# Kernel tuning notes

Hardware: AMD Instinct MI355X
Metric: run time of the kernel (lower is better)

Reference implementation:

```python
import jax, jax.numpy as jnp
import numpy as np

B, C, H, W = 128, 2048, 11, 11
BN_EPS = 1e-5
STEEPNESS = 10.0


def setup_inputs() -> dict:
    key = jax.random.key(0)
    ks = jax.random.split(key, 4)
    x = jax.random.normal(ks[0], (B, C, H, W), dtype=jnp.float32)
    freq_threshold = jnp.full((1, C, 1, 1), 0.25, dtype=jnp.float32)
    gate = jnp.full((1,), 0.1, dtype=jnp.float32)
    # kaiming normal fan_out for 1x1 conv: std = sqrt(2 / fan_out), fan_out = C*1*1
    conv_w = jax.random.normal(ks[1], (C, C), dtype=jnp.float32) * np.sqrt(2.0 / C).astype(np.float32)
    conv_b = jnp.zeros((C,), dtype=jnp.float32)
    bn_gamma = jnp.ones((C,), dtype=jnp.float32)
    bn_beta = jnp.zeros((C,), dtype=jnp.float32)
    bn_mean = jnp.zeros((C,), dtype=jnp.float32)
    bn_var = jnp.ones((C,), dtype=jnp.float32)
    return {
        "x": x, "freq_threshold": freq_threshold, "gate": gate,
        "conv_w": conv_w, "conv_b": conv_b,
        "bn_gamma": bn_gamma, "bn_beta": bn_beta,
        "bn_mean": bn_mean, "bn_var": bn_var,
    }


def _hp_mask(cutoff, h, w, dtype):
    # radial distance from the (shifted) DC bin, normalized by max corner distance
    cy, cx = h // 2, w // 2
    yy = (jnp.arange(h, dtype=dtype) - cy)[:, None]
    xx = (jnp.arange(w, dtype=dtype) - cx)[None, :]
    dist = jnp.sqrt(yy ** 2 + xx ** 2)
    max_dist = jnp.sqrt(jnp.asarray(cy ** 2 + cx ** 2, dtype=dtype))
    dn = dist / (max_dist + 1e-6)  # [H, W]
    return jax.nn.sigmoid(STEEPNESS * (dn[None, None] - cutoff))  # [1, C, H, W]


def reference(x, freq_threshold, gate, conv_w, conv_b, bn_gamma, bn_beta, bn_mean, bn_var):
    # FFT -> shifted high-pass mask -> iFFT (real part)
    x_freq = jnp.fft.fftshift(jnp.fft.fft2(x, norm="ortho"), axes=(-2, -1))
    cutoff = jnp.clip(freq_threshold, 0.05, 0.5)
    mask = _hp_mask(cutoff, x.shape[-2], x.shape[-1], x.dtype)
    x_filt = jnp.fft.ifft2(jnp.fft.ifftshift(x_freq * mask, axes=(-2, -1)), norm="ortho").real
    # refine: 1x1 conv + BN (inference stats) + ReLU
    y = jnp.einsum("bchw,oc->bohw", x_filt, conv_w) + conv_b[None, :, None, None]
    inv = (bn_gamma / jnp.sqrt(bn_var + BN_EPS))[None, :, None, None]
    y = (y - bn_mean[None, :, None, None]) * inv + bn_beta[None, :, None, None]
    y = jax.nn.relu(y)
    g = jnp.clip(gate, 0.0, 1.0)
    return x + g * y
```

## Files before the change

### kernel.cpp

```cpp
#include <hip/hip_runtime.h>
#include <cstdint>
#include <cstddef>


#define C_DIM 2048
#define HW 121
#define NB 128
#define NTOT (NB * HW)

__device__ __forceinline__ unsigned short f2bf(float f) {
  union { float f; unsigned int u; } v;
  v.f = f;
  unsigned int r = (v.u + 0x7FFFu + ((v.u >> 16) & 1u)) >> 16;
  return (unsigned short)r;
}

typedef __bf16 bfrag __attribute__((ext_vector_type(8)));
typedef float f32x4 __attribute__((ext_vector_type(4)));
typedef float f32x2 __attribute__((ext_vector_type(2)));

__device__ __forceinline__ void gload_lds16(const void* g, void* l) {
  __builtin_amdgcn_global_load_lds(
      (const __attribute__((address_space(1))) unsigned int*)(uintptr_t)g,
      (__attribute__((address_space(3))) unsigned int*)(uintptr_t)l, 16, 0, 0);
}

__global__ __launch_bounds__(256) void prep_kernel(
    const float* __restrict__ ft, const float* __restrict__ convb,
    const float* __restrict__ gamma, const float* __restrict__ beta,
    const float* __restrict__ mean, const float* __restrict__ var,
    float* __restrict__ kws, float* __restrict__ alpha,
    float* __restrict__ beta2) {
  __shared__ float msk[121];
  __shared__ float ctab[11];
  const int c = blockIdx.x;
  const int t = threadIdx.x;
  float cutoff = ft[c];
  cutoff = fminf(fmaxf(cutoff, 0.05f), 0.5f);
  if (t < 121) {
    int h = t / 11, w = t - (t / 11) * 11;
    float dy = (float)(h - 5), dx = (float)(w - 5);
    float dn = sqrtf(dy * dy + dx * dx) / (sqrtf(50.0f) + 1e-6f);
    msk[t] = 1.0f / (1.0f + expf(-10.0f * (dn - cutoff)));
  }
  if (t < 11) ctab[t] = cosf(6.283185307179586f * (float)t / 11.0f);
  if (t == 128) {
    float inv = gamma[c] * rsqrtf(var[c] + 1e-5f);
    alpha[c] = inv;
    beta2[c] = (convb[c] - mean[c]) * inv + beta[c];
  }
  __syncthreads();
  if (t < 176) {
    int h = t >> 4, w = t & 15;
    float val = 0.0f;
    if (w < 11) {
      float acc = 0.0f;
      int ru = 0;
      int us = 5;
      for (int u = 0; u < 11; u++) {
        int rv = ru;
        int vs = 5;
        for (int v = 0; v < 11; v++) {
          acc += msk[us * 11 + vs] * ctab[rv];
          rv += w; if (rv >= 11) rv -= 11;
          vs++; if (vs >= 11) vs -= 11;
        }
        ru += h; if (ru >= 11) ru -= 11;
        us++; if (us >= 11) us -= 11;
      }
      val = acc * (1.0f / 121.0f);
    }
    kws[(size_t)c * 176 + t] = val;
  }
}

__global__ __launch_bounds__(256) void wconv_kernel(
    const float* __restrict__ W, unsigned short* __restrict__ Wb) {
  int idx = (blockIdx.x * 256 + threadIdx.x) * 8;
  float4 a = *(const float4*)(W + idx);
  float4 b = *(const float4*)(W + idx + 4);
  union { unsigned short s[8]; uint4 v; } u;
  u.s[0] = f2bf(a.x); u.s[1] = f2bf(a.y); u.s[2] = f2bf(a.z); u.s[3] = f2bf(a.w);
  u.s[4] = f2bf(b.x); u.s[5] = f2bf(b.y); u.s[6] = f2bf(b.z); u.s[7] = f2bf(b.w);
  *(uint4*)(Wb + idx) = u.v;
}

#define XROW 12
#define XPL 132
__global__ __launch_bounds__(704) void filter_kernel(
    const float* __restrict__ x, const float* __restrict__ kws,
    unsigned short* __restrict__ xf) {
  __shared__ __align__(16) float lx[64 * XPL];
  const int b = blockIdx.x;
  const int c0 = blockIdx.y * 64;
  const int tid = threadIdx.x;

  const float* xsrc = x + ((size_t)b * C_DIM + c0) * HW;
#pragma unroll
  for (int i = 0; i < 11; i++) {
    int g = tid + i * 704;
    int pl = g / 121;
    int r = g - pl * 121;
    int rh = r / 11;
    int rw = r - rh * 11;
    lx[pl * XPL + rh * XROW + rw] = xsrc[g];
  }
  __syncthreads();

  const int pl = tid / 11;
  const int ph = tid - pl * 11;
  const float* xp = &lx[pl * XPL];
  const float* kp = kws + (size_t)(c0 + pl) * 176;

  f32x2 acc2[6];
#pragma unroll
  for (int i = 0; i < 6; i++) acc2[i] = f32x2{0.f, 0.f};

  for (int kh = 0; kh < 11; kh++) {
    int qh = ph - kh; if (qh < 0) qh += 11;
    f32x4 xv0 = *(const f32x4*)(xp + qh * XROW);
    f32x4 xv1 = *(const f32x4*)(xp + qh * XROW + 4);
    f32x4 xv2 = *(const f32x4*)(xp + qh * XROW + 8);
    f32x4 kv0 = *(const f32x4*)(kp + kh * 16);
    f32x4 kv1 = *(const f32x4*)(kp + kh * 16 + 4);
    f32x4 kv2 = *(const f32x4*)(kp + kh * 16 + 8);
    const float xr[11] = {xv0[0], xv0[1], xv0[2], xv0[3], xv1[0], xv1[1],
                          xv1[2], xv1[3], xv2[0], xv2[1], xv2[2]};
    float kr[12];
    kr[0] = kv0[0]; kr[1] = kv0[1]; kr[2] = kv0[2]; kr[3] = kv0[3];
    kr[4] = kv1[0]; kr[5] = kv1[1]; kr[6] = kv1[2]; kr[7] = kv1[3];
    kr[8] = kv2[0]; kr[9] = kv2[1]; kr[10] = kv2[2];
    kr[11] = kr[0];
#pragma unroll
    for (int qw = 0; qw < 11; qw++) {
      f32x2 xv = {xr[qw], xr[qw]};
#pragma unroll
      for (int p2 = 0; p2 < 6; p2++) {
        int ki = 2 * p2 - qw; if (ki < 0) ki += 11;
        f32x2 kpair = {kr[ki], kr[ki + 1]};
        acc2[p2] = xv * kpair + acc2[p2];
      }
    }
  }
  __syncthreads();

  float accv[11];
#pragma unroll
  for (int p2 = 0; p2 < 6; p2++) {
    accv[2 * p2] = acc2[p2][0];
    if (2 * p2 + 1 < 11) accv[2 * p2 + 1] = acc2[p2][1];
  }

  unsigned short* lo = (unsigned short*)lx;
#pragma unroll
  for (int pw = 0; pw < 11; pw++)
    lo[(ph * 11 + pw) * 64 + pl] = f2bf(accv[pw]);
  __syncthreads();

  const unsigned int* lou = (const unsigned int*)lo;
#pragma unroll
  for (int i = 0; i < 6; i++) {
    int idx = tid + i * 704;
    if (idx < 3872) {
      int p = idx >> 5;
      int j = idx & 31;
      ((unsigned int*)(xf + (size_t)(b * HW + p) * C_DIM + c0))[j] = lou[idx];
    }
  }
}

__global__ __launch_bounds__(256) void gemm_kernel(
    const unsigned short* __restrict__ Wb, const unsigned short* __restrict__ xf,
    const float* __restrict__ xres, const float* __restrict__ alpha,
    const float* __restrict__ beta2, const float* __restrict__ gate,
    float* __restrict__ out) {
  __shared__ __align__(16) unsigned short lds[16384];
  const int tid = threadIdx.x;
  const int wid = tid >> 6;
  const int lane = tid & 63;

  const int lid = blockIdx.y * 121 + blockIdx.x;
  const int grp = lid / 176;
  const int rem = lid - grp * 176;
  const int m0 = (rem & 15) << 7;
  const int n0 = (grp * 11 + (rem >> 4)) << 7;

  const int wm = (wid >> 1) << 6;
  const int wn = (wid & 1) << 6;

  f32x4 acc[4][4];
#pragma unroll
  for (int i = 0; i < 4; i++)
#pragma unroll
    for (int j = 0; j < 4; j++) acc[i][j] = f32x4{0.f, 0.f, 0.f, 0.f};

  const int rowlo = (wid << 4) + (lane >> 2);
  const int seg = lane & 3;
  const unsigned short* gA0 = Wb + (size_t)(m0 + rowlo) * C_DIM + seg * 8;
  const unsigned short* gA1 = gA0 + 64 * C_DIM;
  const unsigned short* gB0 = xf + (size_t)(n0 + rowlo) * C_DIM + seg * 8;
  const unsigned short* gB1 = gB0 + 64 * C_DIM;
  char* lA0 = (char*)lds + (wid << 10) + (lane << 4);
  char* lA1 = lA0 + 4096;

  const int fr = lane & 15;
  const int quad = lane >> 4;
  const unsigned short* pa = lds + ((wm + fr) << 5) + (quad << 3);
  const unsigned short* pb = lds + 8192 + ((wn + fr) << 5) + (quad << 3);

  for (int kk = 0; kk < 32; kk++) {
    gload_lds16(gA0,       lA0);
    gload_lds16(gA1,       lA1);
    gload_lds16(gA0 + 32,  lA0 + 8192);
    gload_lds16(gA1 + 32,  lA1 + 8192);
    gload_lds16(gB0,       lA0 + 16384);
    gload_lds16(gB1,       lA1 + 16384);
    gload_lds16(gB0 + 32,  lA0 + 24576);
    gload_lds16(gB1 + 32,  lA1 + 24576);
    gA0 += 64; gA1 += 64; gB0 += 64; gB1 += 64;
    asm volatile("s_waitcnt vmcnt(0)" ::: "memory");
    __syncthreads();
#pragma unroll
    for (int ks = 0; ks < 2; ks++) {
      bfrag a[4], b[4];
#pragma unroll
      for (int i = 0; i < 4; i++) {
        a[i] = *(const bfrag*)(pa + (ks << 12) + (i << 9));
        b[i] = *(const bfrag*)(pb + (ks << 12) + (i << 9));
      }
#pragma unroll
      for (int i = 0; i < 4; i++)
#pragma unroll
        for (int j = 0; j < 4; j++)
          acc[i][j] = __builtin_amdgcn_mfma_f32_16x16x32_bf16(a[i], b[j], acc[i][j], 0, 0, 0);
    }
    __syncthreads();
  }

  float g = gate[0];
  g = fminf(fmaxf(g, 0.0f), 1.0f);
  int nbase[4];
#pragma unroll
  for (int j = 0; j < 4; j++) {
    int n = n0 + wn + (j << 4) + fr;
    int bb = n / 121;
    int p = n - bb * 121;
    nbase[j] = bb * (C_DIM * HW) + p;
  }
#pragma unroll
  for (int i = 0; i < 4; i++) {
    const int ob = m0 + wm + (i << 4) + (quad << 2);
    float al[4], bt[4];
#pragma unroll
    for (int r = 0; r < 4; r++) { al[r] = alpha[ob + r]; bt[r] = beta2[ob + r]; }
#pragma unroll
    for (int j = 0; j < 4; j++) {
#pragma unroll
      for (int r = 0; r < 4; r++) {
        int addr = nbase[j] + (ob + r) * HW;
        float v = acc[i][j][r] * al[r] + bt[r];
        v = fmaxf(v, 0.0f);
        out[addr] = xres[addr] + g * v;
      }
    }
  }
}

extern "C" void kernel_launch(void* const* d_in, const int* in_sizes, int n_in,
                              void* d_out, int out_size, void* d_ws, size_t ws_size,
                              hipStream_t stream) {
  const float* x     = (const float*)d_in[0];
  const float* ft    = (const float*)d_in[1];
  const float* gate  = (const float*)d_in[2];
  const float* W     = (const float*)d_in[3];
  const float* convb = (const float*)d_in[4];
  const float* gamma = (const float*)d_in[5];
  const float* beta  = (const float*)d_in[6];
  const float* mean  = (const float*)d_in[7];
  const float* var   = (const float*)d_in[8];
  float* out = (float*)d_out;

  char* ws = (char*)d_ws;
  float* kws            = (float*)(ws);
  float* alpha          = (float*)(ws + 0x200000);
  float* beta2          = (float*)(ws + 0x202000);
  unsigned short* Wb    = (unsigned short*)(ws + 0x300000);
  unsigned short* xf    = (unsigned short*)(ws + 0xC00000);

  prep_kernel<<<2048, 256, 0, stream>>>(ft, convb, gamma, beta, mean, var,
                                        kws, alpha, beta2);
  wconv_kernel<<<2048, 256, 0, stream>>>(W, Wb);
  filter_kernel<<<dim3(NB, C_DIM / 64), 704, 0, stream>>>(x, kws, xf);
  gemm_kernel<<<dim3(NTOT / 128, C_DIM / 128), 256, 0, stream>>>(
      Wb, xf, x, alpha, beta2, gate, out);
}
```

Baseline: 535.3 us.

## Fold weight conversion into prep, exploit kernel symmetry in circular filter

```diff
diff --git a/kernel.cpp b/kernel.cpp
--- a/kernel.cpp
+++ b/kernel.cpp
@@ -17,7 +17,6 @@
 
 typedef __bf16 bfrag __attribute__((ext_vector_type(8)));
 typedef float f32x4 __attribute__((ext_vector_type(4)));
-typedef float f32x2 __attribute__((ext_vector_type(2)));
 
 __device__ __forceinline__ void gload_lds16(const void* g, void* l) {
   __builtin_amdgcn_global_load_lds(
@@ -29,12 +28,24 @@
     const float* __restrict__ ft, const float* __restrict__ convb,
     const float* __restrict__ gamma, const float* __restrict__ beta,
     const float* __restrict__ mean, const float* __restrict__ var,
+    const float* __restrict__ W, unsigned short* __restrict__ Wb,
     float* __restrict__ kws, float* __restrict__ alpha,
     float* __restrict__ beta2) {
   __shared__ float msk[121];
   __shared__ float ctab[11];
   const int c = blockIdx.x;
   const int t = threadIdx.x;
+
+  {
+    int base = c * C_DIM + t * 8;
+    float4 a = *(const float4*)(W + base);
+    float4 b = *(const float4*)(W + base + 4);
+    union { unsigned short s[8]; uint4 v; } u;
+    u.s[0] = f2bf(a.x); u.s[1] = f2bf(a.y); u.s[2] = f2bf(a.z); u.s[3] = f2bf(a.w);
+    u.s[4] = f2bf(b.x); u.s[5] = f2bf(b.y); u.s[6] = f2bf(b.z); u.s[7] = f2bf(b.w);
+    *(uint4*)(Wb + base) = u.v;
+  }
+
   float cutoff = ft[c];
   cutoff = fminf(fmaxf(cutoff, 0.05f), 0.5f);
   if (t < 121) {
@@ -74,96 +85,89 @@
   }
 }
 
-__global__ __launch_bounds__(256) void wconv_kernel(
-    const float* __restrict__ W, unsigned short* __restrict__ Wb) {
-  int idx = (blockIdx.x * 256 + threadIdx.x) * 8;
-  float4 a = *(const float4*)(W + idx);
-  float4 b = *(const float4*)(W + idx + 4);
-  union { unsigned short s[8]; uint4 v; } u;
-  u.s[0] = f2bf(a.x); u.s[1] = f2bf(a.y); u.s[2] = f2bf(a.z); u.s[3] = f2bf(a.w);
-  u.s[4] = f2bf(b.x); u.s[5] = f2bf(b.y); u.s[6] = f2bf(b.z); u.s[7] = f2bf(b.w);
-  *(uint4*)(Wb + idx) = u.v;
-}
-
 #define XROW 12
 #define XPL 132
-__global__ __launch_bounds__(704) void filter_kernel(
+#define FC 32
+__global__ __launch_bounds__(384) void filter_kernel(
     const float* __restrict__ x, const float* __restrict__ kws,
     unsigned short* __restrict__ xf) {
-  __shared__ __align__(16) float lx[64 * XPL];
+  __shared__ __align__(16) float lx[FC * XPL];
+  __shared__ __align__(16) unsigned short lo[HW * FC];
   const int b = blockIdx.x;
-  const int c0 = blockIdx.y * 64;
+  const int c0 = blockIdx.y * FC;
   const int tid = threadIdx.x;
 
   const float* xsrc = x + ((size_t)b * C_DIM + c0) * HW;
 #pragma unroll
-  for (int i = 0; i < 11; i++) {
-    int g = tid + i * 704;
-    int pl = g / 121;
-    int r = g - pl * 121;
-    int rh = r / 11;
-    int rw = r - rh * 11;
-    lx[pl * XPL + rh * XROW + rw] = xsrc[g];
+  for (int i = 0; i < 3; i++) {
+    int v = tid + i * 384;
+    if (v < 968) {
+      float4 xv = *(const float4*)(xsrc + v * 4);
+      int g = v * 4;
+#pragma unroll
+      for (int e = 0; e < 4; e++) {
+        int ge = g + e;
+        int pl = ge / 121;
+        int r = ge - pl * 121;
+        int rh = r / 11;
+        int rw = r - rh * 11;
+        lx[pl * XPL + rh * XROW + rw] = (&xv.x)[e];
+      }
+    }
   }
   __syncthreads();
 
-  const int pl = tid / 11;
-  const int ph = tid - pl * 11;
-  const float* xp = &lx[pl * XPL];
-  const float* kp = kws + (size_t)(c0 + pl) * 176;
-
-  f32x2 acc2[6];
-#pragma unroll
-  for (int i = 0; i < 6; i++) acc2[i] = f32x2{0.f, 0.f};
-
-  for (int kh = 0; kh < 11; kh++) {
-    int qh = ph - kh; if (qh < 0) qh += 11;
-    f32x4 xv0 = *(const f32x4*)(xp + qh * XROW);
-    f32x4 xv1 = *(const f32x4*)(xp + qh * XROW + 4);
-    f32x4 xv2 = *(const f32x4*)(xp + qh * XROW + 8);
-    f32x4 kv0 = *(const f32x4*)(kp + kh * 16);
-    f32x4 kv1 = *(const f32x4*)(kp + kh * 16 + 4);
-    f32x4 kv2 = *(const f32x4*)(kp + kh * 16 + 8);
-    const float xr[11] = {xv0[0], xv0[1], xv0[2], xv0[3], xv1[0], xv1[1],
-                          xv1[2], xv1[3], xv2[0], xv2[1], xv2[2]};
-    float kr[12];
-    kr[0] = kv0[0]; kr[1] = kv0[1]; kr[2] = kv0[2]; kr[3] = kv0[3];
-    kr[4] = kv1[0]; kr[5] = kv1[1]; kr[6] = kv1[2]; kr[7] = kv1[3];
-    kr[8] = kv2[0]; kr[9] = kv2[1]; kr[10] = kv2[2];
-    kr[11] = kr[0];
-#pragma unroll
-    for (int qw = 0; qw < 11; qw++) {
-      f32x2 xv = {xr[qw], xr[qw]};
-#pragma unroll
-      for (int p2 = 0; p2 < 6; p2++) {
-        int ki = 2 * p2 - qw; if (ki < 0) ki += 11;
-        f32x2 kpair = {kr[ki], kr[ki + 1]};
-        acc2[p2] = xv * kpair + acc2[p2];
-      }
-    }
+  if (tid < 352) {
+    const int pl = tid / 11;
+    const int ph = tid - pl * 11;
+    const float* xp = &lx[pl * XPL];
+    const float* kp = kws + (size_t)(c0 + pl) * 176;
+
+    float accv[11];
+#pragma unroll
+    for (int i = 0; i < 11; i++) accv[i] = 0.f;
+
+#pragma unroll
+    for (int d = 0; d <= 5; d++) {
+      int q0 = ph - d; if (q0 < 0) q0 += 11;
+      f32x4 r0 = *(const f32x4*)(xp + q0 * XROW);
+      f32x4 r1 = *(const f32x4*)(xp + q0 * XROW + 4);
+      f32x4 r2 = *(const f32x4*)(xp + q0 * XROW + 8);
+      if (d > 0) {
+        int q1 = ph + d; if (q1 >= 11) q1 -= 11;
+        r0 += *(const f32x4*)(xp + q1 * XROW);
+        r1 += *(const f32x4*)(xp + q1 * XROW + 4);
+        r2 += *(const f32x4*)(xp + q1 * XROW + 8);
+      }
+      const float R[11] = {r0[0], r0[1], r0[2], r0[3], r1[0], r1[1],
+                           r1[2], r1[3], r2[0], r2[1], r2[2]};
+      f32x4 k0 = *(const f32x4*)(kp + d * 16);
+      f32x4 k1 = *(const f32x4*)(kp + d * 16 + 4);
+      f32x4 k2 = *(const f32x4*)(kp + d * 16 + 8);
+      const float K[11] = {k0[0], k0[1], k0[2], k0[3], k1[0], k1[1],
+                           k1[2], k1[3], k2[0], k2[1], k2[2]};
+#pragma unroll
+      for (int qw = 0; qw < 11; qw++) {
+#pragma unroll
+        for (int pw = 0; pw < 11; pw++) {
+          int ki = pw - qw; if (ki < 0) ki += 11;
+          accv[pw] = fmaf(R[qw], K[ki], accv[pw]);
+        }
+      }
+    }
+#pragma unroll
+    for (int pw = 0; pw < 11; pw++)
+      lo[(ph * 11 + pw) * FC + pl] = f2bf(accv[pw]);
   }
   __syncthreads();
 
-  float accv[11];
-#pragma unroll
-  for (int p2 = 0; p2 < 6; p2++) {
-    accv[2 * p2] = acc2[p2][0];
-    if (2 * p2 + 1 < 11) accv[2 * p2 + 1] = acc2[p2][1];
-  }
-
-  unsigned short* lo = (unsigned short*)lx;
-#pragma unroll
-  for (int pw = 0; pw < 11; pw++)
-    lo[(ph * 11 + pw) * 64 + pl] = f2bf(accv[pw]);
-  __syncthreads();
-
   const unsigned int* lou = (const unsigned int*)lo;
 #pragma unroll
   for (int i = 0; i < 6; i++) {
-    int idx = tid + i * 704;
-    if (idx < 3872) {
-      int p = idx >> 5;
-      int j = idx & 31;
+    int idx = tid + i * 384;
+    if (idx < 1936) {
+      int p = idx >> 4;
+      int j = idx & 15;
       ((unsigned int*)(xf + (size_t)(b * HW + p) * C_DIM + c0))[j] = lou[idx];
     }
   }
@@ -288,9 +292,8 @@
   unsigned short* xf    = (unsigned short*)(ws + 0xC00000);
 
   prep_kernel<<<2048, 256, 0, stream>>>(ft, convb, gamma, beta, mean, var,
-                                        kws, alpha, beta2);
-  wconv_kernel<<<2048, 256, 0, stream>>>(W, Wb);
-  filter_kernel<<<dim3(NB, C_DIM / 64), 704, 0, stream>>>(x, kws, xf);
+                                        W, Wb, kws, alpha, beta2);
+  filter_kernel<<<dim3(NB, C_DIM / FC), 384, 0, stream>>>(x, kws, xf);
   gemm_kernel<<<dim3(NTOT / 128, C_DIM / 128), 256, 0, stream>>>(
       Wb, xf, x, alpha, beta2, gate, out);
 }
```

After: 468.5 us. 1.14x faster.
